# Kernel tuning notes

Hardware: AMD Instinct MI355X
Metric: run time of the kernel (lower is better)

Reference implementation:

```python
import jax, jax.numpy as jnp
import numpy as np

L = 8        # num_layers
B = 4        # batch
S = 1024     # seq_len
D = 1024     # hidden_size
H = 16       # num_heads
FC = 4096    # fc_size
NEG = -1e9   # additive causal-mask value (matches torch code's -1000000000.0)


def setup_inputs() -> dict:
    key = jax.random.key(0)
    ks = jax.random.split(key, 12)
    std = 0.02
    inputs = jax.random.normal(ks[0], (B, S, D), jnp.float32)
    # per-layer stacked parameters; torch Linear y = x W^T + b, here stored as [in, out]
    Wq = jax.random.normal(ks[1], (L, D, D), jnp.float32) * std
    Wk = jax.random.normal(ks[2], (L, D, D), jnp.float32) * std
    Wv = jax.random.normal(ks[3], (L, D, D), jnp.float32) * std
    Wo = jax.random.normal(ks[4], (L, D, D), jnp.float32) * std
    W1 = jax.random.normal(ks[5], (L, D, FC), jnp.float32) * std
    W2 = jax.random.normal(ks[6], (L, FC, D), jnp.float32) * std
    bq = jnp.zeros((L, D), jnp.float32)
    bk = jnp.zeros((L, D), jnp.float32)
    bv = jnp.zeros((L, D), jnp.float32)
    bo = jnp.zeros((L, D), jnp.float32)
    b1 = jnp.zeros((L, FC), jnp.float32)
    b2 = jnp.zeros((L, D), jnp.float32)
    ln_g = jnp.ones((D,), jnp.float32)   # single LayerNorm shared across all sites
    ln_b = jnp.zeros((D,), jnp.float32)
    scale = jnp.asarray(0.1, jnp.float32)  # re-zero residual scale (init 0 in torch; 0.1 for non-degenerate test)
    return dict(inputs=inputs, Wq=Wq, bq=bq, Wk=Wk, bk=bk, Wv=Wv, bv=bv,
                Wo=Wo, bo=bo, W1=W1, b1=b1, W2=W2, b2=b2,
                ln_g=ln_g, ln_b=ln_b, scale=scale)


def reference(inputs, Wq, bq, Wk, bk, Wv, bv, Wo, bo, W1, b1, W2, b2, ln_g, ln_b, scale):
    Bz, Sl, Dm = inputs.shape
    nL = Wq.shape[0]
    dh = Dm // H
    inv_sqrt_dh = 1.0 / np.sqrt(dh).astype(np.float32)

    def layer_norm(x):  # shared gamma/beta, eps matches torch default 1e-5
        mu = jnp.mean(x, axis=-1, keepdims=True)
        var = jnp.var(x, axis=-1, keepdims=True)
        return (x - mu) * jax.lax.rsqrt(var + 1e-5) * ln_g + ln_b

    # causal additive bias [S, S], broadcasts over [B, H, S, S]
    bias = jnp.triu(jnp.full((Sl, Sl), NEG, inputs.dtype), k=1)

    x = inputs
    for i in range(nL):
        # --- masked self-attention block ---
        r = layer_norm(x)
        q = (r @ Wq[i] + bq[i]).reshape(Bz, Sl, H, dh)
        k = (r @ Wk[i] + bk[i]).reshape(Bz, Sl, H, dh)
        v = (r @ Wv[i] + bv[i]).reshape(Bz, Sl, H, dh)
        logits = jnp.einsum('bqhd,bkhd->bhqk', q, k) * inv_sqrt_dh + bias
        attn = jax.nn.softmax(logits, axis=-1)
        vals = jnp.einsum('bhqk,bkhd->bqhd', attn, v).reshape(Bz, Sl, Dm)
        r = vals @ Wo[i] + bo[i]
        x = x + scale * r  # re-zero residual (dropout is identity at inference)
        # --- FFN block ---
        r = layer_norm(x)
        r = jax.nn.gelu(r @ W1[i] + b1[i], approximate=False) @ W2[i] + b2[i]
        x = x + scale * r
    return layer_norm(x)
```

## Files before the change

kernel.cpp:

```cpp
#include <hip/hip_runtime.h>


typedef __bf16 bf16x8 __attribute__((ext_vector_type(8)));
typedef float  f32x4  __attribute__((ext_vector_type(4)));

#define DEV static __device__ __forceinline__

DEV unsigned short f2bf(float x) {
  unsigned u = __builtin_bit_cast(unsigned int, x);
  u += 0x7fffu + ((u >> 16) & 1u);
  return (unsigned short)(u >> 16);
}

DEV f32x4 mfma16(bf16x8 a, bf16x8 b, f32x4 c) {
  return __builtin_amdgcn_mfma_f32_16x16x32_bf16(a, b, c, 0, 0, 0);
}

DEV bf16x8 ldb8(const unsigned short* p) {
  return *reinterpret_cast<const bf16x8*>(p);
}

DEV void gload_lds16(const unsigned short* g, unsigned short* l) {
  __builtin_amdgcn_global_load_lds(
      (const __attribute__((address_space(1))) void*)g,
      (__attribute__((address_space(3))) void*)l, 16, 0, 0);
}

__global__ void transpose_cvt(const float* __restrict__ src,
                              unsigned short* __restrict__ dst,
                              int srcStride, int dstStride) {
  __shared__ float tile[32][33];
  const int t  = threadIdx.x;
  const int r  = t >> 3;
  const int c4 = (t & 7) << 2;
  const int k  = blockIdx.x * 32 + r;
  const int n0 = blockIdx.y * 32 + c4;
  const float4 v = *reinterpret_cast<const float4*>(src + (size_t)k * srcStride + n0);
  tile[r][c4] = v.x; tile[r][c4 + 1] = v.y; tile[r][c4 + 2] = v.z; tile[r][c4 + 3] = v.w;
  __syncthreads();
  const int n  = blockIdx.y * 32 + r;
  const int k0 = blockIdx.x * 32 + c4;
  ushort4 o;
  o.x = f2bf(tile[c4][r]);     o.y = f2bf(tile[c4 + 1][r]);
  o.z = f2bf(tile[c4 + 2][r]); o.w = f2bf(tile[c4 + 3][r]);
  *reinterpret_cast<ushort4*>(dst + (size_t)n * dstStride + k0) = o;
}

__global__ void transpose_cvt4(const float* __restrict__ Wq, const float* __restrict__ Wk,
                               const float* __restrict__ Wv, const float* __restrict__ Wo,
                               unsigned short* __restrict__ Wqkv_t,
                               unsigned short* __restrict__ Wo_t) {
  __shared__ float tile[32][33];
  const int z = blockIdx.z;
  const float* src = (z == 0) ? Wq : (z == 1) ? Wk : (z == 2) ? Wv : Wo;
  unsigned short* dst = (z == 3) ? Wo_t : (Wqkv_t + (size_t)z * 1024 * 1024);
  const int t  = threadIdx.x;
  const int r  = t >> 3;
  const int c4 = (t & 7) << 2;
  const int k  = blockIdx.x * 32 + r;
  const int n0 = blockIdx.y * 32 + c4;
  const float4 v = *reinterpret_cast<const float4*>(src + (size_t)k * 1024 + n0);
  tile[r][c4] = v.x; tile[r][c4 + 1] = v.y; tile[r][c4 + 2] = v.z; tile[r][c4 + 3] = v.w;
  __syncthreads();
  const int n  = blockIdx.y * 32 + r;
  const int k0 = blockIdx.x * 32 + c4;
  ushort4 o;
  o.x = f2bf(tile[c4][r]);     o.y = f2bf(tile[c4 + 1][r]);
  o.z = f2bf(tile[c4 + 2][r]); o.w = f2bf(tile[c4 + 3][r]);
  *reinterpret_cast<ushort4*>(dst + (size_t)n * 1024 + k0) = o;
}

__global__ void pack_qkv_bias(const float* __restrict__ bq, const float* __restrict__ bk,
                              const float* __restrict__ bv, float* __restrict__ out) {
  int i = blockIdx.x * 256 + threadIdx.x;
  out[i] = (i < 1024) ? bq[i] : (i < 2048 ? bk[i - 1024] : bv[i - 2048]);
}

template <int OUTF32>
__global__ __launch_bounds__(256) void ln_kernel(
    const float* x, const float* __restrict__ gam,
    const float* __restrict__ bet, void* out) {
  const int t = threadIdx.x, wave = t >> 6, lane = t & 63;
  const int row = blockIdx.x * 4 + wave;
  const float* xr = x + (size_t)row * 1024;
  float4 v[4];
  float s = 0.f, ss = 0.f;
  #pragma unroll
  for (int k = 0; k < 4; ++k) {
    v[k] = *reinterpret_cast<const float4*>(xr + k * 256 + lane * 4);
    s  += v[k].x + v[k].y + v[k].z + v[k].w;
    ss += v[k].x * v[k].x + v[k].y * v[k].y + v[k].z * v[k].z + v[k].w * v[k].w;
  }
  #pragma unroll
  for (int m = 1; m <= 32; m <<= 1) { s += __shfl_xor(s, m); ss += __shfl_xor(ss, m); }
  const float mean = s * (1.0f / 1024.0f);
  const float var  = ss * (1.0f / 1024.0f) - mean * mean;
  const float rstd = rsqrtf(var + 1e-5f);
  #pragma unroll
  for (int k = 0; k < 4; ++k) {
    const float4 g  = *reinterpret_cast<const float4*>(gam + k * 256 + lane * 4);
    const float4 bb = *reinterpret_cast<const float4*>(bet + k * 256 + lane * 4);
    const float y0 = (v[k].x - mean) * rstd * g.x + bb.x;
    const float y1 = (v[k].y - mean) * rstd * g.y + bb.y;
    const float y2 = (v[k].z - mean) * rstd * g.z + bb.z;
    const float y3 = (v[k].w - mean) * rstd * g.w + bb.w;
    if (OUTF32) {
      float4 o; o.x = y0; o.y = y1; o.z = y2; o.w = y3;
      *reinterpret_cast<float4*>((float*)out + (size_t)row * 1024 + k * 256 + lane * 4) = o;
    } else {
      ushort4 o; o.x = f2bf(y0); o.y = f2bf(y1); o.z = f2bf(y2); o.w = f2bf(y3);
      *reinterpret_cast<ushort4*>((unsigned short*)out + (size_t)row * 1024 + k * 256 + lane * 4) = o;
    }
  }
}

template <int MODE>
__global__ __launch_bounds__(512) void gemm8r(
    const unsigned short* __restrict__ A, const unsigned short* __restrict__ Bt,
    const float* __restrict__ bias, unsigned short* __restrict__ outb,
    unsigned short* __restrict__ vT, int N, int K) {
  __shared__ __attribute__((aligned(16))) unsigned short lds[7 * 8192];
  const int t = threadIdx.x, wave = t >> 6, lane = t & 63;
  const int wm = wave >> 2, wn = wave & 3;
  const int rl15 = lane & 15;

  const int nbn = N >> 8;
  const int qq  = gridDim.x >> 3;
  const int swz = (blockIdx.x & 7) * qq + (blockIdx.x >> 3);
  const int m0 = (swz / nbn) << 8, n0 = (swz % nbn) << 8;

  const unsigned short* aG = A  + (size_t)m0 * K;
  const unsigned short* bG = Bt + (size_t)n0 * K;

  const int srow = lane >> 2;
  const int ssl  = (((lane & 3) ^ ((srow >> 1) & 3)) << 3);
  const int swA  = (((lane >> 4) ^ ((lane >> 1) & 3)) << 3);

  auto stageA = [&](int slot, int kt) {
    #pragma unroll
    for (int j = 0; j < 2; ++j) {
      const int c = wave + j * 8;
      gload_lds16(aG + (size_t)(c * 16 + srow) * K + kt * 32 + ssl,
                  &lds[slot * 8192 + c * 512]);
    }
  };
  auto stageB = [&](int slot, int kt) {
    #pragma unroll
    for (int j = 0; j < 2; ++j) {
      const int c = wave + j * 8;
      gload_lds16(bG + (size_t)(c * 16 + srow) * K + kt * 32 + ssl,
                  &lds[slot * 8192 + c * 512]);
    }
  };

  const int nk = K >> 5;
  stageA(0, 0); stageB(1, 0);
  stageA(2, 1); stageB(3, 1);
  asm volatile("s_waitcnt vmcnt(4)" ::: "memory");
  asm volatile("s_barrier" ::: "memory");

  f32x4 acc[8][4] = {};
  int sA = 0, sB = 1, pA = 4, pB = 5;

  for (int kt = 0; kt < nk; ++kt) {
    const bool more = (kt + 2 < nk);
    if (more) { stageA(pA, kt + 2); stageB(pB, kt + 2); }
    const int ab = sA * 8192, bb = sB * 8192;
    bf16x8 af[8], bfr[4];
    #pragma unroll
    for (int mi = 0; mi < 8; ++mi)
      af[mi] = ldb8(&lds[ab + (wm * 128 + mi * 16 + rl15) * 32 + swA]);
    #pragma unroll
    for (int ni = 0; ni < 4; ++ni)
      bfr[ni] = ldb8(&lds[bb + (wn * 64 + ni * 16 + rl15) * 32 + swA]);
    __builtin_amdgcn_s_setprio(1);
    #pragma unroll
    for (int mi = 0; mi < 8; ++mi)
      #pragma unroll
      for (int ni = 0; ni < 4; ++ni)
        acc[mi][ni] = mfma16(af[mi], bfr[ni], acc[mi][ni]);
    __builtin_amdgcn_s_setprio(0);
    if (more) asm volatile("s_waitcnt vmcnt(4)" ::: "memory");
    else      asm volatile("s_waitcnt vmcnt(0)" ::: "memory");
    asm volatile("s_barrier" ::: "memory");
    sA += 2; if (sA >= 7) sA -= 7;
    sB += 2; if (sB >= 7) sB -= 7;
    pA += 2; if (pA >= 7) pA -= 7;
    pB += 2; if (pB >= 7) pB -= 7;
  }

  const int mrow = m0 + wm * 128 + (lane >> 4) * 4;
  const int ncol = n0 + wn * 64 + rl15;
  #pragma unroll
  for (int ni = 0; ni < 4; ++ni) {
    const int n = ncol + ni * 16;
    const float bn = bias[n];
    #pragma unroll
    for (int mi = 0; mi < 8; ++mi) {
      const int row0 = mrow + mi * 16;
      if constexpr (MODE == 3) {
        if (n >= 2048) {
          const int h = (n - 2048) >> 6, d = (n - 2048) & 63;
          const int b = row0 >> 10, s = row0 & 1023;
          ushort4 o;
          o.x = f2bf(acc[mi][ni][0] + bn); o.y = f2bf(acc[mi][ni][1] + bn);
          o.z = f2bf(acc[mi][ni][2] + bn); o.w = f2bf(acc[mi][ni][3] + bn);
          *reinterpret_cast<ushort4*>(vT + ((size_t)(b * 16 + h) * 64 + d) * 1024 + s) = o;
          continue;
        }
      }
      #pragma unroll
      for (int r = 0; r < 4; ++r) {
        const size_t idx = (size_t)(row0 + r) * N + n;
        float v = acc[mi][ni][r] + bn;
        if constexpr (MODE == 1)
          v = 0.5f * v * (1.0f + erff(v * 0.70710678118f));
        outb[idx] = f2bf(v);
      }
    }
  }
}

template <int MODE, int BN>
__global__ __launch_bounds__(256) void gemm2(
    const unsigned short* __restrict__ A, const unsigned short* __restrict__ Bt,
    const float* __restrict__ bias, unsigned short* __restrict__ outb,
    const float* xin, float* xout, const float* __restrict__ scale_p,
    int N, int K) {
  constexpr int NI = BN / 32;
  constexpr int BSH = BN * 64;
  __shared__ __attribute__((aligned(16))) unsigned short lds[2][8192 + BSH];
  const int t = threadIdx.x, wave = t >> 6, lane = t & 63;
  const int m0 = blockIdx.x * 128, n0 = blockIdx.y * BN;
  const int wm = wave >> 1, wn = wave & 1;

  int srowA[4], scolA[4];
  #pragma unroll
  for (int j = 0; j < 4; ++j) {
    const int c = j * 256 + wave * 64 + lane;
    const int r = c >> 3;
    srowA[j] = r;
    scolA[j] = ((c & 7) ^ (r & 7)) << 3;
  }
  const unsigned short* aBase = A + (size_t)m0 * K;
  const unsigned short* bBase = Bt + (size_t)n0 * K;

  const int xk0 = (((lane >> 4)    ) ^ (lane & 7)) << 3;
  const int xk1 = (((lane >> 4) | 4) ^ (lane & 7)) << 3;
  const int arow = (wm * 64 + (lane & 15)) * 64;
  const int brow = (wn * (BN / 2) + (lane & 15)) * 64;

  f32x4 acc[4][NI] = {};
  const int nk = K >> 6;
  constexpr int BJ = NI;

  {
    unsigned short* l = &lds[0][0];
    #pragma unroll
    for (int j = 0; j < 4; ++j)
      gload_lds16(aBase + (size_t)srowA[j] * K + scolA[j], l + j * 2048 + wave * 512);
    #pragma unroll
    for (int j = 0; j < BJ; ++j)
      gload_lds16(bBase + (size_t)srowA[j] * K + scolA[j], l + 8192 + j * 2048 + wave * 512);
  }
  __syncthreads();

  int cur = 0;
  for (int kt = 0; kt < nk; ++kt) {
    if (kt + 1 < nk) {
      unsigned short* l = &lds[cur ^ 1][0];
      const int ko = (kt + 1) * 64;
      #pragma unroll
      for (int j = 0; j < 4; ++j)
        gload_lds16(aBase + (size_t)srowA[j] * K + ko + scolA[j], l + j * 2048 + wave * 512);
      #pragma unroll
      for (int j = 0; j < BJ; ++j)
        gload_lds16(bBase + (size_t)srowA[j] * K + ko + scolA[j], l + 8192 + j * 2048 + wave * 512);
    }
    const unsigned short* l = &lds[cur][0];
    #pragma unroll
    for (int kc = 0; kc < 2; ++kc) {
      const int xk = kc ? xk1 : xk0;
      bf16x8 a[4], b[NI];
      #pragma unroll
      for (int mi = 0; mi < 4; ++mi) a[mi] = ldb8(&l[arow + mi * 1024 + xk]);
      #pragma unroll
      for (int ni = 0; ni < NI; ++ni) b[ni] = ldb8(&l[8192 + brow + ni * 1024 + xk]);
      __builtin_amdgcn_s_setprio(1);
      #pragma unroll
      for (int mi = 0; mi < 4; ++mi)
        #pragma unroll
        for (int ni = 0; ni < NI; ++ni)
          acc[mi][ni] = mfma16(a[mi], b[ni], acc[mi][ni]);
      __builtin_amdgcn_s_setprio(0);
    }
    __syncthreads();
    cur ^= 1;
  }

  const int mrow = m0 + wm * 64 + (lane >> 4) * 4;
  const int ncol = n0 + wn * (BN / 2) + (lane & 15);
  float scl = 0.f;
  if constexpr (MODE == 2) scl = scale_p[0];
  #pragma unroll
  for (int ni = 0; ni < NI; ++ni) {
    const int n = ncol + ni * 16;
    const float bn = bias[n];
    #pragma unroll
    for (int mi = 0; mi < 4; ++mi) {
      #pragma unroll
      for (int r = 0; r < 4; ++r) {
        const size_t idx = (size_t)(mrow + mi * 16 + r) * N + n;
        float v = acc[mi][ni][r] + bn;
        if constexpr (MODE == 1) {
          v = 0.5f * v * (1.0f + erff(v * 0.70710678118f));
          outb[idx] = f2bf(v);
        } else if constexpr (MODE == 2) {
          xout[idx] = xin[idx] + scl * v;
        } else {
          outb[idx] = f2bf(v);
        }
      }
    }
  }
}

__global__ __launch_bounds__(256) void attn_kernel(
    const unsigned short* __restrict__ qkv, const unsigned short* __restrict__ vT,
    unsigned short* __restrict__ vals) {
  const int bh = blockIdx.x & 63;
  const int g  = 15 - (blockIdx.x >> 6);
  const int b = bh >> 4, h = bh & 15;
  const int t = threadIdx.x, wave = t >> 6, lane = t & 63;
  const int rowLane = lane & 15, grp = lane >> 4;
  const int qt = g * 4 + wave;
  const int q0 = qt * 16;
  const int nkt = (qt >> 2) + 1;

  __shared__ __attribute__((aligned(16))) unsigned short P_lds[4][16 * 72];
  unsigned short* P = P_lds[wave];

  const unsigned short* qkvB  = qkv + (size_t)b * 1024 * 3072;
  const unsigned short* kBase = qkvB + 1024 + h * 64 + grp * 8;
  const unsigned short* vHead = vT + (size_t)bh * 64 * 1024;

  const unsigned short* qb = qkvB + (size_t)(q0 + rowLane) * 3072 + h * 64 + grp * 8;
  const bf16x8 aq0 = ldb8(qb);
  const bf16x8 aq1 = ldb8(qb + 32);

  f32x4 oacc[4] = {};
  float mrun = -1e30f, lrun = 0.f;

  bf16x8 k0[4], k1[4];
  #pragma unroll
  for (int nf = 0; nf < 4; ++nf) {
    const unsigned short* kb = kBase + (size_t)(nf * 16 + rowLane) * 3072;
    k0[nf] = ldb8(kb); k1[nf] = ldb8(kb + 32);
  }

  for (int kt = 0; kt < nkt; ++kt) {
    const int kv0 = kt * 64;
    bf16x8 v0[4], v1[4];
    #pragma unroll
    for (int df = 0; df < 4; ++df) {
      const unsigned short* vb = vHead + (size_t)(df * 16 + rowLane) * 1024 + kv0 + grp * 8;
      v0[df] = ldb8(vb); v1[df] = ldb8(vb + 32);
    }
    f32x4 sacc[4];
    #pragma unroll
    for (int nf = 0; nf < 4; ++nf) {
      f32x4 z = {0.f, 0.f, 0.f, 0.f};
      z = mfma16(k0[nf], aq0, z);
      z = mfma16(k1[nf], aq1, z);
      sacc[nf] = z;
    }
    if (kt + 1 < nkt) {
      #pragma unroll
      for (int nf = 0; nf < 4; ++nf) {
        const unsigned short* kb = kBase + (size_t)(kv0 + 64 + nf * 16 + rowLane) * 3072;
        k0[nf] = ldb8(kb); k1[nf] = ldb8(kb + 32);
      }
    }
    float pl[4][4];
    #pragma unroll
    for (int nf = 0; nf < 4; ++nf)
      #pragma unroll
      for (int r = 0; r < 4; ++r) pl[nf][r] = sacc[nf][r] * 0.125f;
    if (kt == nkt - 1) {
      const int qg = q0 + rowLane;
      #pragma unroll
      for (int nf = 0; nf < 4; ++nf)
        #pragma unroll
        for (int r = 0; r < 4; ++r)
          if (kv0 + nf * 16 + grp * 4 + r > qg) pl[nf][r] = -1e30f;
    }
    float mloc = pl[0][0];
    #pragma unroll
    for (int nf = 0; nf < 4; ++nf)
      #pragma unroll
      for (int r = 0; r < 4; ++r) mloc = fmaxf(mloc, pl[nf][r]);
    mloc = fmaxf(mloc, __shfl_xor(mloc, 16));
    mloc = fmaxf(mloc, __shfl_xor(mloc, 32));
    const float mnew = fmaxf(mrun, mloc);
    const float facq = __expf(mrun - mnew);
    mrun = mnew;
    float sloc = 0.f;
    #pragma unroll
    for (int nf = 0; nf < 4; ++nf)
      #pragma unroll
      for (int r = 0; r < 4; ++r) {
        const float e = __expf(pl[nf][r] - mnew);
        pl[nf][r] = e;
        sloc += e;
      }
    sloc += __shfl_xor(sloc, 16);
    sloc += __shfl_xor(sloc, 32);
    lrun = lrun * facq + sloc;
    float fac_r[4];
    #pragma unroll
    for (int r = 0; r < 4; ++r) fac_r[r] = __shfl(facq, grp * 4 + r);
    #pragma unroll
    for (int df = 0; df < 4; ++df)
      #pragma unroll
      for (int r = 0; r < 4; ++r) oacc[df][r] *= fac_r[r];
    #pragma unroll
    for (int nf = 0; nf < 4; ++nf)
      #pragma unroll
      for (int r = 0; r < 4; ++r)
        P[rowLane * 72 + nf * 16 + grp * 4 + r] = f2bf(pl[nf][r]);
    const bf16x8 pa0 = ldb8(&P[rowLane * 72 + grp * 8]);
    const bf16x8 pa1 = ldb8(&P[rowLane * 72 + 32 + grp * 8]);
    #pragma unroll
    for (int df = 0; df < 4; ++df) {
      oacc[df] = mfma16(pa0, v0[df], oacc[df]);
      oacc[df] = mfma16(pa1, v1[df], oacc[df]);
    }
  }
  const float rlq = 1.0f / lrun;
  float rl[4];
  #pragma unroll
  for (int r = 0; r < 4; ++r) rl[r] = __shfl(rlq, grp * 4 + r);
  #pragma unroll
  for (int df = 0; df < 4; ++df)
    #pragma unroll
    for (int r = 0; r < 4; ++r) {
      const int qg = q0 + grp * 4 + r;
      const float v = oacc[df][r] * rl[r];
      vals[(size_t)(b * 1024 + qg) * 1024 + h * 64 + df * 16 + rowLane] = f2bf(v);
    }
}

extern "C" void kernel_launch(void* const* d_in, const int* in_sizes, int n_in,
                              void* d_out, int out_size, void* d_ws, size_t ws_size,
                              hipStream_t stream) {
  (void)in_sizes; (void)n_in; (void)out_size; (void)ws_size;
  const float* inputs = (const float*)d_in[0];
  const float* Wq = (const float*)d_in[1];  const float* bq = (const float*)d_in[2];
  const float* Wk = (const float*)d_in[3];  const float* bk = (const float*)d_in[4];
  const float* Wv = (const float*)d_in[5];  const float* bv = (const float*)d_in[6];
  const float* Wo = (const float*)d_in[7];  const float* bo = (const float*)d_in[8];
  const float* W1 = (const float*)d_in[9];  const float* b1 = (const float*)d_in[10];
  const float* W2 = (const float*)d_in[11]; const float* b2 = (const float*)d_in[12];
  const float* ln_g = (const float*)d_in[13];
  const float* ln_b = (const float*)d_in[14];
  const float* scale_p = (const float*)d_in[15];
  float* xbuf = (float*)d_out;

  char* w = (char*)d_ws;
  size_t off = 0;
  auto take = [&](size_t bytes) {
    void* p = w + off;
    off = (off + bytes + 255) & ~(size_t)255;
    return p;
  };
  unsigned short* Wqkv_t = (unsigned short*)take((size_t)3072 * 1024 * 2);
  unsigned short* Wo_t   = (unsigned short*)take((size_t)1024 * 1024 * 2);
  unsigned short* W1_t   = (unsigned short*)take((size_t)4096 * 1024 * 2);
  unsigned short* W2_t   = (unsigned short*)take((size_t)1024 * 4096 * 2);
  float*          bqkv   = (float*)take(3072 * 4);
  unsigned short* rbuf   = (unsigned short*)take((size_t)4096 * 1024 * 2);
  unsigned short* qkvb   = (unsigned short*)take((size_t)4096 * 3072 * 2);
  unsigned short* vTb    = (unsigned short*)take((size_t)64 * 64 * 1024 * 2);
  unsigned short* valsb  = (unsigned short*)take((size_t)4096 * 1024 * 2);
  unsigned short* hbuf   = (unsigned short*)take((size_t)4096 * 4096 * 2);

  for (int i = 0; i < 8; ++i) {
    const float* xin = (i == 0) ? inputs : xbuf;
    transpose_cvt4<<<dim3(32, 32, 4), 256, 0, stream>>>(
        Wq + (size_t)i * 1024 * 1024, Wk + (size_t)i * 1024 * 1024,
        Wv + (size_t)i * 1024 * 1024, Wo + (size_t)i * 1024 * 1024, Wqkv_t, Wo_t);
    transpose_cvt<<<dim3(32, 128), 256, 0, stream>>>(W1 + (size_t)i * 1024 * 4096, W1_t, 4096, 1024);
    transpose_cvt<<<dim3(128, 32), 256, 0, stream>>>(W2 + (size_t)i * 4096 * 1024, W2_t, 1024, 4096);
    pack_qkv_bias<<<12, 256, 0, stream>>>(bq + i * 1024, bk + i * 1024, bv + i * 1024, bqkv);
    ln_kernel<0><<<1024, 256, 0, stream>>>(xin, ln_g, ln_b, rbuf);
    gemm8r<3><<<192, 512, 0, stream>>>(rbuf, Wqkv_t, bqkv, qkvb, vTb, 3072, 1024);
    attn_kernel<<<1024, 256, 0, stream>>>(qkvb, vTb, valsb);
    gemm2<2, 64><<<dim3(32, 16), 256, 0, stream>>>(valsb, Wo_t, bo + i * 1024, nullptr,
                                                   xin, xbuf, scale_p, 1024, 1024);
    ln_kernel<0><<<1024, 256, 0, stream>>>(xbuf, ln_g, ln_b, rbuf);
    gemm8r<1><<<256, 512, 0, stream>>>(rbuf, W1_t, b1 + i * 4096, hbuf, nullptr, 4096, 1024);
    gemm2<2, 64><<<dim3(32, 16), 256, 0, stream>>>(hbuf, W2_t, b2 + i * 1024, nullptr,
                                                   xbuf, xbuf, scale_p, 1024, 4096);
  }
  ln_kernel<1><<<1024, 256, 0, stream>>>(xbuf, ln_g, ln_b, xbuf);
}
```

Measured before the change: 2.087 ms.

## Restructure attention with LDS-staged shared K/V tiles and 32x32 MFMA

Rewrites the causal attention kernel so each block handles 128 query rows, with 32 rows per wave. K and V tiles are staged into double-buffered, XOR-swizzled LDS through global_load_lds and shared by all four waves, instead of each wave loading K/V from global memory itself. It switches to 32x32x16 MFMAs and builds the P operand with cross-lane shuffles instead of an LDS round trip. The goal is less redundant global traffic and fewer instructions per FLOP, at the cost of half as many blocks, per-tile block barriers, and waves sitting idle on tiles past their diagonal.

```diff
diff --git a/kernel.cpp b/kernel.cpp
--- a/kernel.cpp
+++ b/kernel.cpp
@@ -3,6 +3,8 @@
 
 typedef __bf16 bf16x8 __attribute__((ext_vector_type(8)));
 typedef float  f32x4  __attribute__((ext_vector_type(4)));
+typedef float  f32x16 __attribute__((ext_vector_type(16)));
+typedef unsigned int u32x4 __attribute__((ext_vector_type(4)));
 
 #define DEV static __device__ __forceinline__
 
@@ -12,8 +14,16 @@
   return (unsigned short)(u >> 16);
 }
 
+DEV unsigned int pack2bf(float lo, float hi) {
+  return (unsigned int)f2bf(lo) | ((unsigned int)f2bf(hi) << 16);
+}
+
 DEV f32x4 mfma16(bf16x8 a, bf16x8 b, f32x4 c) {
   return __builtin_amdgcn_mfma_f32_16x16x32_bf16(a, b, c, 0, 0, 0);
+}
+
+DEV f32x16 mfma32(bf16x8 a, bf16x8 b, f32x16 c) {
+  return __builtin_amdgcn_mfma_f32_32x32x16_bf16(a, b, c, 0, 0, 0);
 }
 
 DEV bf16x8 ldb8(const unsigned short* p) {
@@ -329,124 +339,131 @@
     const unsigned short* __restrict__ qkv, const unsigned short* __restrict__ vT,
     unsigned short* __restrict__ vals) {
   const int bh = blockIdx.x & 63;
-  const int g  = 15 - (blockIdx.x >> 6);
+  const int qb = 7 - (blockIdx.x >> 6);
   const int b = bh >> 4, h = bh & 15;
   const int t = threadIdx.x, wave = t >> 6, lane = t & 63;
-  const int rowLane = lane & 15, grp = lane >> 4;
-  const int qt = g * 4 + wave;
-  const int q0 = qt * 16;
-  const int nkt = (qt >> 2) + 1;
-
-  __shared__ __attribute__((aligned(16))) unsigned short P_lds[4][16 * 72];
-  unsigned short* P = P_lds[wave];
+  const int l31 = lane & 31, hi = lane >> 5;
+  const int q0w = qb * 128 + wave * 32;
+  const int diag = q0w >> 6;
+  const int nkt = qb * 2 + 2;
+
+  __shared__ __attribute__((aligned(16))) unsigned short ldsK[2][4096];
+  __shared__ __attribute__((aligned(16))) unsigned short ldsV[2][4096];
 
   const unsigned short* qkvB  = qkv + (size_t)b * 1024 * 3072;
-  const unsigned short* kBase = qkvB + 1024 + h * 64 + grp * 8;
   const unsigned short* vHead = vT + (size_t)bh * 64 * 1024;
 
-  const unsigned short* qb = qkvB + (size_t)(q0 + rowLane) * 3072 + h * 64 + grp * 8;
-  const bf16x8 aq0 = ldb8(qb);
-  const bf16x8 aq1 = ldb8(qb + 32);
-
-  f32x4 oacc[4] = {};
+  const int c0row = t >> 3, c0ch = t & 7;
+  const int c1row = (t + 256) >> 3, c1ch = t & 7;
+  const int s0col = ((c0ch ^ (c0row & 7)) << 3);
+  const int s1col = ((c1ch ^ (c1row & 7)) << 3);
+  const int wbase = (t >> 6) * 512;
+
+  auto stageKV = [&](int buf, int kt) {
+    const int kv0 = kt * 64;
+    gload_lds16(qkvB + (size_t)(kv0 + c0row) * 3072 + 1024 + h * 64 + s0col,
+                &ldsK[buf][wbase]);
+    gload_lds16(qkvB + (size_t)(kv0 + c1row) * 3072 + 1024 + h * 64 + s1col,
+                &ldsK[buf][2048 + wbase]);
+    gload_lds16(vHead + (size_t)c0row * 1024 + kv0 + s0col, &ldsV[buf][wbase]);
+    gload_lds16(vHead + (size_t)c1row * 1024 + kv0 + s1col, &ldsV[buf][2048 + wbase]);
+  };
+
+  const unsigned short* qrow = qkvB + (size_t)(q0w + l31) * 3072 + h * 64 + hi * 8;
+  bf16x8 qf[4];
+  #pragma unroll
+  for (int s = 0; s < 4; ++s) qf[s] = ldb8(qrow + 16 * s);
+
+  f32x16 oacc[2] = {};
   float mrun = -1e30f, lrun = 0.f;
 
-  bf16x8 k0[4], k1[4];
-  #pragma unroll
-  for (int nf = 0; nf < 4; ++nf) {
-    const unsigned short* kb = kBase + (size_t)(nf * 16 + rowLane) * 3072;
-    k0[nf] = ldb8(kb); k1[nf] = ldb8(kb + 32);
-  }
+  stageKV(0, 0);
+  __syncthreads();
 
   for (int kt = 0; kt < nkt; ++kt) {
-    const int kv0 = kt * 64;
-    bf16x8 v0[4], v1[4];
-    #pragma unroll
-    for (int df = 0; df < 4; ++df) {
-      const unsigned short* vb = vHead + (size_t)(df * 16 + rowLane) * 1024 + kv0 + grp * 8;
-      v0[df] = ldb8(vb); v1[df] = ldb8(vb + 32);
-    }
-    f32x4 sacc[4];
-    #pragma unroll
-    for (int nf = 0; nf < 4; ++nf) {
-      f32x4 z = {0.f, 0.f, 0.f, 0.f};
-      z = mfma16(k0[nf], aq0, z);
-      z = mfma16(k1[nf], aq1, z);
-      sacc[nf] = z;
-    }
-    if (kt + 1 < nkt) {
-      #pragma unroll
-      for (int nf = 0; nf < 4; ++nf) {
-        const unsigned short* kb = kBase + (size_t)(kv0 + 64 + nf * 16 + rowLane) * 3072;
-        k0[nf] = ldb8(kb); k1[nf] = ldb8(kb + 32);
+    const int cur = kt & 1;
+    if (kt + 1 < nkt) stageKV(cur ^ 1, kt + 1);
+    if (kt <= diag) {
+      const unsigned short* K = ldsK[cur];
+      const unsigned short* V = ldsV[cur];
+      #pragma unroll
+      for (int sub = 0; sub < 2; ++sub) {
+        const int krow = sub * 32 + l31;
+        f32x16 sacc = {};
+        #pragma unroll
+        for (int s = 0; s < 4; ++s) {
+          const bf16x8 kf = ldb8(&K[krow * 64 + (((2 * s + hi) ^ (krow & 7)) << 3)]);
+          sacc = mfma32(kf, qf[s], sacc);
+        }
+        float p[16];
+        #pragma unroll
+        for (int r = 0; r < 16; ++r) p[r] = sacc[r] * 0.125f;
+        if (kt == diag) {
+          const int qg = q0w + l31;
+          #pragma unroll
+          for (int r = 0; r < 16; ++r) {
+            const int kv = kt * 64 + sub * 32 + (r & 3) + 8 * (r >> 2) + 4 * hi;
+            if (kv > qg) p[r] = -1e30f;
+          }
+        }
+        float mloc = p[0];
+        #pragma unroll
+        for (int r = 1; r < 16; ++r) mloc = fmaxf(mloc, p[r]);
+        mloc = fmaxf(mloc, __shfl_xor(mloc, 32));
+        const float mnew = fmaxf(mrun, mloc);
+        const float facq = __expf(mrun - mnew);
+        mrun = mnew;
+        float sloc = 0.f;
+        #pragma unroll
+        for (int r = 0; r < 16; ++r) {
+          const float e = __expf(p[r] - mnew);
+          p[r] = e;
+          sloc += e;
+        }
+        sloc += __shfl_xor(sloc, 32);
+        lrun = lrun * facq + sloc;
+        #pragma unroll
+        for (int db = 0; db < 2; ++db)
+          #pragma unroll
+          for (int r = 0; r < 16; ++r) oacc[db][r] *= facq;
+        unsigned int w[8], x[8];
+        #pragma unroll
+        for (int i = 0; i < 8; ++i) w[i] = pack2bf(p[2 * i], p[2 * i + 1]);
+        #pragma unroll
+        for (int i = 0; i < 8; ++i) x[i] = (unsigned)__shfl_xor((int)w[i], 32);
+        #pragma unroll
+        for (int ks = 0; ks < 2; ++ks) {
+          const int qi = 2 * ks + hi;
+          u32x4 fu;
+          if (hi) { fu = u32x4{x[2 * qi], x[2 * qi + 1], w[2 * qi], w[2 * qi + 1]}; }
+          else    { fu = u32x4{w[2 * qi], w[2 * qi + 1], x[2 * qi], x[2 * qi + 1]}; }
+          const bf16x8 pf = __builtin_bit_cast(bf16x8, fu);
+          #pragma unroll
+          for (int db = 0; db < 2; ++db) {
+            const int vrow = db * 32 + l31;
+            const int vch  = sub * 4 + ks * 2 + hi;
+            const bf16x8 vf = ldb8(&V[vrow * 64 + ((vch ^ (vrow & 7)) << 3)]);
+            oacc[db] = mfma32(vf, pf, oacc[db]);
+          }
+        }
       }
     }
-    float pl[4][4];
-    #pragma unroll
-    for (int nf = 0; nf < 4; ++nf)
-      #pragma unroll
-      for (int r = 0; r < 4; ++r) pl[nf][r] = sacc[nf][r] * 0.125f;
-    if (kt == nkt - 1) {
-      const int qg = q0 + rowLane;
-      #pragma unroll
-      for (int nf = 0; nf < 4; ++nf)
-        #pragma unroll
-        for (int r = 0; r < 4; ++r)
-          if (kv0 + nf * 16 + grp * 4 + r > qg) pl[nf][r] = -1e30f;
-    }
-    float mloc = pl[0][0];
-    #pragma unroll
-    for (int nf = 0; nf < 4; ++nf)
-      #pragma unroll
-      for (int r = 0; r < 4; ++r) mloc = fmaxf(mloc, pl[nf][r]);
-    mloc = fmaxf(mloc, __shfl_xor(mloc, 16));
-    mloc = fmaxf(mloc, __shfl_xor(mloc, 32));
-    const float mnew = fmaxf(mrun, mloc);
-    const float facq = __expf(mrun - mnew);
-    mrun = mnew;
-    float sloc = 0.f;
-    #pragma unroll
-    for (int nf = 0; nf < 4; ++nf)
-      #pragma unroll
-      for (int r = 0; r < 4; ++r) {
-        const float e = __expf(pl[nf][r] - mnew);
-        pl[nf][r] = e;
-        sloc += e;
-      }
-    sloc += __shfl_xor(sloc, 16);
-    sloc += __shfl_xor(sloc, 32);
-    lrun = lrun * facq + sloc;
-    float fac_r[4];
-    #pragma unroll
-    for (int r = 0; r < 4; ++r) fac_r[r] = __shfl(facq, grp * 4 + r);
-    #pragma unroll
-    for (int df = 0; df < 4; ++df)
-      #pragma unroll
-      for (int r = 0; r < 4; ++r) oacc[df][r] *= fac_r[r];
-    #pragma unroll
-    for (int nf = 0; nf < 4; ++nf)
-      #pragma unroll
-      for (int r = 0; r < 4; ++r)
-        P[rowLane * 72 + nf * 16 + grp * 4 + r] = f2bf(pl[nf][r]);
-    const bf16x8 pa0 = ldb8(&P[rowLane * 72 + grp * 8]);
-    const bf16x8 pa1 = ldb8(&P[rowLane * 72 + 32 + grp * 8]);
-    #pragma unroll
-    for (int df = 0; df < 4; ++df) {
-      oacc[df] = mfma16(pa0, v0[df], oacc[df]);
-      oacc[df] = mfma16(pa1, v1[df], oacc[df]);
-    }
-  }
-  const float rlq = 1.0f / lrun;
-  float rl[4];
-  #pragma unroll
-  for (int r = 0; r < 4; ++r) rl[r] = __shfl(rlq, grp * 4 + r);
-  #pragma unroll
-  for (int df = 0; df < 4; ++df)
-    #pragma unroll
-    for (int r = 0; r < 4; ++r) {
-      const int qg = q0 + grp * 4 + r;
-      const float v = oacc[df][r] * rl[r];
-      vals[(size_t)(b * 1024 + qg) * 1024 + h * 64 + df * 16 + rowLane] = f2bf(v);
+    __syncthreads();
+  }
+
+  const float rl = 1.0f / lrun;
+  const size_t qrowOut = (size_t)(b * 1024 + q0w + l31) * 1024 + h * 64;
+  #pragma unroll
+  for (int db = 0; db < 2; ++db)
+    #pragma unroll
+    for (int rq = 0; rq < 4; ++rq) {
+      const int d0 = db * 32 + 8 * rq + 4 * hi;
+      ushort4 o;
+      o.x = f2bf(oacc[db][rq * 4 + 0] * rl);
+      o.y = f2bf(oacc[db][rq * 4 + 1] * rl);
+      o.z = f2bf(oacc[db][rq * 4 + 2] * rl);
+      o.w = f2bf(oacc[db][rq * 4 + 3] * rl);
+      *reinterpret_cast<ushort4*>(vals + qrowOut + d0) = o;
     }
 }
 
@@ -494,7 +511,7 @@
     pack_qkv_bias<<<12, 256, 0, stream>>>(bq + i * 1024, bk + i * 1024, bv + i * 1024, bqkv);
     ln_kernel<0><<<1024, 256, 0, stream>>>(xin, ln_g, ln_b, rbuf);
     gemm8r<3><<<192, 512, 0, stream>>>(rbuf, Wqkv_t, bqkv, qkvb, vTb, 3072, 1024);
-    attn_kernel<<<1024, 256, 0, stream>>>(qkvb, vTb, valsb);
+    attn_kernel<<<512, 256, 0, stream>>>(qkvb, vTb, valsb);
     gemm2<2, 64><<<dim3(32, 16), 256, 0, stream>>>(valsb, Wo_t, bo + i * 1024, nullptr,
                                                    xin, xbuf, scale_p, 1024, 1024);
     ln_kernel<0><<<1024, 256, 0, stream>>>(xbuf, ln_g, ln_b, rbuf);
```

After: 1.846 ms. -11.5%, faster.
